# Kernel tuning notes

Measured on AMD Instinct MI355X. Metric: run time of the kernel, lower is better.

The kernel has to match this reference:

```python
import jax, jax.numpy as jnp
import numpy as np

D_HID = 1024
N_HEADS = 16
D_HEAD = D_HID // N_HEADS


def setup_inputs() -> dict:
    key = jax.random.key(0)
    k_x, k_w, k_b = jax.random.split(key, 3)
    x = jax.random.normal(k_x, (8, 4096, D_HID), dtype=jnp.float32)
    # qkv linear params (torch Linear: y = x @ W.T + b; we store W already transposed)
    W_qkv = jax.random.normal(k_w, (D_HID, 3 * D_HID), dtype=jnp.float32) / np.sqrt(D_HID)
    b_qkv = jax.random.normal(k_b, (3 * D_HID,), dtype=jnp.float32) * 0.01
    return {"x": x, "W_qkv": W_qkv, "b_qkv": b_qkv}


def reference(x, W_qkv, b_qkv):
    B, N, _ = x.shape
    qkv = x @ W_qkv + b_qkv  # [B, N, 3*d_hid]
    q, k, v = jnp.split(qkv, 3, axis=-1)

    def heads(t):  # [B, N, d_hid] -> [B, H, N, d_head]
        return t.reshape(B, N, N_HEADS, D_HEAD).transpose(0, 2, 1, 3)

    q, k, v = heads(q), heads(k), heads(v)
    # channel attention: contract over sequence N -> [B, H, d_head, d_head]
    attn = jnp.einsum("bhnd,bhne->bhde", q, k) / np.sqrt(D_HEAD)
    attn = jax.nn.softmax(attn, axis=-1)  # softmax over channel dim
    # outputs = V @ attn : [B, H, N, d_head]
    out = jnp.einsum("bhnd,bhde->bhne", v, attn)
    out = out.transpose(0, 2, 1, 3).reshape(B, N, N_HEADS * D_HEAD)
    return out
```

## Files before the change

### kernel.cpp

```cpp
#include <hip/hip_runtime.h>
#include <hip/hip_bf16.h>


typedef __attribute__((ext_vector_type(4))) float  f32x4;
typedef __attribute__((ext_vector_type(8))) short  bf16x8;
typedef __attribute__((ext_vector_type(8))) unsigned short u16x8;

typedef __attribute__((address_space(1))) const unsigned int GBUF;
typedef __attribute__((address_space(3))) unsigned int       LBUF;

#define DEVI __device__ __forceinline__

static constexpr int BATCH = 8;
static constexpr int NSEQ  = 4096;
static constexpr int DHID  = 1024;
static constexpr int NHEAD = 16;
static constexpr int DH    = 64;
static constexpr int MROWS = BATCH * NSEQ;
static constexpr int N3    = 3 * DHID;

DEVI unsigned short f2bf(float f) {
    unsigned int u = __float_as_uint(f);
    u = (u + 0x7fffu + ((u >> 16) & 1u)) >> 16;
    return (unsigned short)u;
}

__global__ void k_cvt_x(const float* __restrict__ x, unsigned short* __restrict__ xb, int n8) {
    int i = blockIdx.x * 256 + threadIdx.x;
    int stride = gridDim.x * 256;
    for (; i < n8; i += stride) {
        f32x4 a = *(const f32x4*)(x + (size_t)i * 8);
        f32x4 b = *(const f32x4*)(x + (size_t)i * 8 + 4);
        u16x8 r;
#pragma unroll
        for (int j = 0; j < 4; j++) { r[j] = f2bf(a[j]); r[4 + j] = f2bf(b[j]); }
        *(u16x8*)(xb + (size_t)i * 8) = r;
    }
}

__global__ void k_wt(const float* __restrict__ W, unsigned short* __restrict__ Wt) {
    __shared__ float s[32][33];
    int c0 = blockIdx.x * 32;
    int k0 = blockIdx.y * 32;
    int tx = threadIdx.x & 31, ty = threadIdx.x >> 5;
#pragma unroll
    for (int i = 0; i < 4; i++)
        s[ty + 8 * i][tx] = W[(size_t)(k0 + ty + 8 * i) * N3 + c0 + tx];
    __syncthreads();
#pragma unroll
    for (int i = 0; i < 4; i++)
        Wt[(size_t)(c0 + ty + 8 * i) * DHID + k0 + tx] = f2bf(s[tx][ty + 8 * i]);
}

__global__ __launch_bounds__(512, 2) void k_gemm1(
        const unsigned short* __restrict__ xb, const unsigned short* __restrict__ Wt,
        const float* __restrict__ bias,
        unsigned short* __restrict__ Q, unsigned short* __restrict__ Kw,
        unsigned short* __restrict__ V) {
    __shared__ __align__(16) unsigned short As[2][16384];
    __shared__ __align__(16) unsigned short Bs[2][16384];

    int nwg = gridDim.x;
    int cpx = nwg >> 3;
    int id  = blockIdx.x;
    int swz = (id & 7) * cpx + (id >> 3);
    int mt = swz / 12, nt = swz % 12;
    int m0 = mt * 256, n0 = nt * 256;

    int t = threadIdx.x, l = t & 63, w = t >> 6;
    int wr = w >> 2, wc = w & 3;
    int lr = l & 15;

    const unsigned short* aSrc = xb + (size_t)m0 * DHID;
    const unsigned short* bSrc = Wt + (size_t)n0 * DHID;

    int scol = ((t & 7) * 8) ^ (((t >> 3) & 7) << 3);
    int c0 = ((l >> 4) * 8) ^ ((l & 7) << 3);
    int aRow = wr * 128 + lr;
    int bRow = wc * 64 + lr;

#define STAGE_A(bi, kt, h) do { \
        const unsigned short* _s = aSrc + (size_t)((h) * 128 + (t >> 3)) * DHID + (kt) * 64 + scol; \
        unsigned short* _d = &As[bi][(h) * 8192 + t * 8]; \
        __builtin_amdgcn_global_load_lds((GBUF*)_s, (LBUF*)_d, 16, 0, 0); \
        __builtin_amdgcn_global_load_lds((GBUF*)(_s + 64 * DHID), (LBUF*)(_d + 4096), 16, 0, 0); \
    } while (0)
#define STAGE_B(bi, kt, h) do { \
        const unsigned short* _s = bSrc + (size_t)((h) * 128 + (t >> 3)) * DHID + (kt) * 64 + scol; \
        unsigned short* _d = &Bs[bi][(h) * 8192 + t * 8]; \
        __builtin_amdgcn_global_load_lds((GBUF*)_s, (LBUF*)_d, 16, 0, 0); \
        __builtin_amdgcn_global_load_lds((GBUF*)(_s + 64 * DHID), (LBUF*)(_d + 4096), 16, 0, 0); \
    } while (0)
#define LDA(bi, dst, mh) \
    _Pragma("unroll") for (int m2 = 0; m2 < 4; m2++) { \
        const unsigned short* _row = &As[bi][(aRow + (mh) * 64 + m2 * 16) * 64]; \
        dst[m2][0] = *(const bf16x8*)(_row + c0); \
        dst[m2][1] = *(const bf16x8*)(_row + (c0 ^ 32)); \
    }
#define LDB(bi, dst, nh) \
    _Pragma("unroll") for (int n2 = 0; n2 < 2; n2++) { \
        const unsigned short* _row = &Bs[bi][(bRow + (nh) * 32 + n2 * 16) * 64]; \
        dst[n2][0] = *(const bf16x8*)(_row + c0); \
        dst[n2][1] = *(const bf16x8*)(_row + (c0 ^ 32)); \
    }
#define MM(mh, nh, A_, B_) \
    _Pragma("unroll") for (int m2 = 0; m2 < 4; m2++) \
    _Pragma("unroll") for (int n2 = 0; n2 < 2; n2++) { \
        acc[(mh)*4+m2][(nh)*2+n2] = __builtin_amdgcn_mfma_f32_16x16x32_bf16(A_[m2][0], B_[n2][0], acc[(mh)*4+m2][(nh)*2+n2], 0, 0, 0); \
        acc[(mh)*4+m2][(nh)*2+n2] = __builtin_amdgcn_mfma_f32_16x16x32_bf16(A_[m2][1], B_[n2][1], acc[(mh)*4+m2][(nh)*2+n2], 0, 0, 0); \
    }
#define BAR __builtin_amdgcn_s_barrier()
#define LGKM0 do { asm volatile("s_waitcnt lgkmcnt(0)" ::: "memory"); \
                   __builtin_amdgcn_sched_barrier(0); } while (0)
#define VM4 asm volatile("s_waitcnt vmcnt(4)" ::: "memory")
#define VM0 asm volatile("s_waitcnt vmcnt(0)" ::: "memory")
#define PRIO1 __builtin_amdgcn_s_setprio(1)
#define PRIO0 __builtin_amdgcn_s_setprio(0)

    f32x4 acc[8][4] = {};
    bf16x8 fA0[4][2], fA1[4][2], fB0[2][2], fB1[2][2];

    STAGE_A(0, 0, 0); STAGE_A(0, 0, 1);
    STAGE_B(0, 0, 0); STAGE_B(0, 0, 1);
    STAGE_A(1, 1, 0); STAGE_A(1, 1, 1);
    VM4;
    BAR;

#pragma unroll 1
    for (int i = 0; i < 8; ++i) {
        int kc1 = 2 * i + 1;
        int kn0 = (2 * i + 2) & 15, kn1 = (2 * i + 3) & 15;
        LDA(0, fA0, 0); LDB(0, fB0, 0); STAGE_B(1, kc1, 0);
        BAR; LGKM0; PRIO1; MM(0, 0, fA0, fB0); PRIO0; BAR;

        LDA(0, fA1, 1); STAGE_B(1, kc1, 1);
        BAR; LGKM0; PRIO1; MM(1, 0, fA1, fB0); PRIO0; BAR;

        LDB(0, fB1, 1); STAGE_A(0, kn0, 0);
        BAR; LGKM0; PRIO1; MM(1, 1, fA1, fB1); PRIO0; BAR;

        STAGE_A(0, kn0, 1);
        BAR; PRIO1; MM(0, 1, fA0, fB1); PRIO0;
        VM4;
        BAR;
        LDA(1, fA0, 0); LDB(1, fB0, 0); STAGE_B(0, kn0, 0);
        BAR; LGKM0; PRIO1; MM(0, 0, fA0, fB0); PRIO0; BAR;

        LDA(1, fA1, 1); STAGE_B(0, kn0, 1);
        BAR; LGKM0; PRIO1; MM(1, 0, fA1, fB0); PRIO0; BAR;

        LDB(1, fB1, 1); STAGE_A(1, kn1, 0);
        BAR; LGKM0; PRIO1; MM(1, 1, fA1, fB1); PRIO0; BAR;

        STAGE_A(1, kn1, 1);
        BAR; PRIO1; MM(0, 1, fA0, fB1); PRIO0;
        VM4;
        BAR;
    }

    VM0;
    BAR;

    int hg   = nt * 4 + wc;
    int part = hg >> 4;
    int h    = hg & 15;
    unsigned short* dst = (part == 0) ? Q : ((part == 1) ? Kw : V);
    int b   = m0 >> 12;
    int nnb = m0 & 4095;
    unsigned short* dstp = dst + ((size_t)(b * 16 + h) * NSEQ) * DH;

    unsigned short* eb = (w < 4) ? (&As[0][0] + w * 8192) : (&Bs[0][0] + (w - 4) * 8192);

    float bv[4];
#pragma unroll
    for (int n = 0; n < 4; n++) bv[n] = bias[n0 + wc * 64 + n * 16 + lr];

#pragma unroll
    for (int n = 0; n < 4; n++)
#pragma unroll
        for (int m = 0; m < 8; m++)
#pragma unroll
            for (int j = 0; j < 4; j++) {
                int lm = m * 16 + (l >> 4) * 4 + j;
                eb[lm * 64 + ((n * 16 + lr) ^ (((lm >> 2) & 3) << 4))] =
                    f2bf(acc[m][n][j] + bv[n]);
            }

    const size_t base2 = (size_t)(nnb + wr * 128) * DH;
#pragma unroll
    for (int rr = 0; rr < 16; rr++) {
        int u = rr * 64 + l;
        int row = u >> 3, unit = u & 7;
        bf16x8 v = *(const bf16x8*)&eb[row * 64 + ((unit * 8) ^ (((row >> 2) & 3) << 4))];
        *(bf16x8*)(dstp + base2 + (size_t)u * 8) = v;
    }
#undef STAGE_A
#undef STAGE_B
#undef LDA
#undef LDB
#undef MM
#undef BAR
#undef LGKM0
#undef VM4
#undef VM0
#undef PRIO1
#undef PRIO0
}

__global__ __launch_bounds__(256, 2) void k_qk(
        const unsigned short* __restrict__ Q, const unsigned short* __restrict__ K,
        float* __restrict__ part) {
    __shared__ unsigned short Qt[64 * 40];
    __shared__ unsigned short Kt[64 * 40];

    int bid = blockIdx.x;
    int bh = bid >> 2, ch = bid & 3;
    const unsigned short* Qb = Q + ((size_t)bh * NSEQ + ch * 1024) * DH;
    const unsigned short* Kb = K + ((size_t)bh * NSEQ + ch * 1024) * DH;

    int t = threadIdx.x, l = t & 63, w = t >> 6;
    int wr = w >> 1, wc = w & 1;
    int nn = t & 31;
    int dg = t >> 5;

    f32x4 acc[2][2] = {};

    size_t ro0 = (size_t)nn * DH + dg * 8;
    bf16x8 qv = *(const bf16x8*)(Qb + ro0);
    bf16x8 kv = *(const bf16x8*)(Kb + ro0);

    for (int ns = 0; ns < 32; ns++) {
        const size_t rn = (size_t)((((ns + 1) & 31) * 32) + nn) * DH + dg * 8;
        bf16x8 qn = *(const bf16x8*)(Qb + rn);
        bf16x8 kn = *(const bf16x8*)(Kb + rn);
        __syncthreads();
#pragma unroll
        for (int j = 0; j < 8; j++) {
            Qt[(dg * 8 + j) * 40 + nn] = qv[j];
            Kt[(dg * 8 + j) * 40 + nn] = kv[j];
        }
        __syncthreads();
        bf16x8 a[2], b[2];
#pragma unroll
        for (int m = 0; m < 2; m++)
            a[m] = *(const bf16x8*)(Qt + (wr * 32 + m * 16 + (l & 15)) * 40 + (l >> 4) * 8);
#pragma unroll
        for (int n = 0; n < 2; n++)
            b[n] = *(const bf16x8*)(Kt + (wc * 32 + n * 16 + (l & 15)) * 40 + (l >> 4) * 8);
#pragma unroll
        for (int m = 0; m < 2; m++)
#pragma unroll
            for (int n = 0; n < 2; n++)
                acc[m][n] = __builtin_amdgcn_mfma_f32_16x16x32_bf16(a[m], b[n], acc[m][n], 0, 0, 0);
        qv = qn; kv = kn;
    }

    float* P = part + ((size_t)ch * 128 + bh) * 4096;
#pragma unroll
    for (int m = 0; m < 2; m++)
#pragma unroll
        for (int n = 0; n < 2; n++)
#pragma unroll
            for (int j = 0; j < 4; j++) {
                int d = wr * 32 + m * 16 + (l >> 4) * 4 + j;
                int e = wc * 32 + n * 16 + (l & 15);
                P[d * 64 + e] = acc[m][n][j];
            }
}

__global__ void k_softmax(const float* __restrict__ part, unsigned short* __restrict__ attn_t) {
    int bh = blockIdx.x;
    int d  = threadIdx.x;
    const float* p = part + (size_t)bh * 4096 + d * 64;
    const size_t cs = (size_t)128 * 4096;
    float s[64];
#pragma unroll
    for (int e = 0; e < 64; e++)
        s[e] = (p[e] + p[cs + e] + p[2 * cs + e] + p[3 * cs + e]) * 0.125f;
    float mx = s[0];
#pragma unroll
    for (int e = 1; e < 64; e++) mx = fmaxf(mx, s[e]);
    float sum = 0.f;
#pragma unroll
    for (int e = 0; e < 64; e++) { s[e] = __expf(s[e] - mx); sum += s[e]; }
    float inv = 1.f / sum;
    unsigned short* a = attn_t + (size_t)bh * 4096;
#pragma unroll
    for (int e = 0; e < 64; e++)
        a[e * 64 + d] = f2bf(s[e] * inv);
}

__global__ __launch_bounds__(256, 2) void k_out(
        const unsigned short* __restrict__ V, const unsigned short* __restrict__ attn_t,
        float* __restrict__ out) {
    int bid = blockIdx.x;
    int bh = bid >> 4, ntile = bid & 15;
    int b = bh >> 4, h = bh & 15;
    int t = threadIdx.x, l = t & 63, w = t >> 6;
    int r0 = ntile * 256 + w * 64;

    const unsigned short* Vb = V + (size_t)bh * NSEQ * DH;
    const unsigned short* Ab = attn_t + (size_t)bh * 4096;

    bf16x8 bf[4][2];
#pragma unroll
    for (int n = 0; n < 4; n++)
#pragma unroll
        for (int ks = 0; ks < 2; ks++)
            bf[n][ks] = *(const bf16x8*)(Ab + (n * 16 + (l & 15)) * 64 + ks * 32 + (l >> 4) * 8);

    f32x4 acc[4][4] = {};
#pragma unroll
    for (int m = 0; m < 4; m++) {
        const unsigned short* vr = Vb + (size_t)(r0 + m * 16 + (l & 15)) * DH + (l >> 4) * 8;
        bf16x8 av0 = *(const bf16x8*)(vr);
        bf16x8 av1 = *(const bf16x8*)(vr + 32);
#pragma unroll
        for (int n = 0; n < 4; n++) {
            acc[m][n] = __builtin_amdgcn_mfma_f32_16x16x32_bf16(av0, bf[n][0], acc[m][n], 0, 0, 0);
            acc[m][n] = __builtin_amdgcn_mfma_f32_16x16x32_bf16(av1, bf[n][1], acc[m][n], 0, 0, 0);
        }
    }

    float* ob = out + (size_t)b * NSEQ * DHID + (size_t)h * DH;
#pragma unroll
    for (int m = 0; m < 4; m++)
#pragma unroll
        for (int n = 0; n < 4; n++)
#pragma unroll
            for (int j = 0; j < 4; j++) {
                int nn = r0 + m * 16 + (l >> 4) * 4 + j;
                int e  = n * 16 + (l & 15);
                ob[(size_t)nn * DHID + e] = acc[m][n][j];
            }
}

extern "C" void kernel_launch(void* const* d_in, const int* in_sizes, int n_in,
                              void* d_out, int out_size, void* d_ws, size_t ws_size,
                              hipStream_t stream) {
    const float* x    = (const float*)d_in[0];
    const float* W    = (const float*)d_in[1];
    const float* bias = (const float*)d_in[2];
    float* out = (float*)d_out;

    char* wsp = (char*)d_ws;
    unsigned short* xb   = (unsigned short*)(wsp);
    unsigned short* Wt   = (unsigned short*)(wsp + 67108864);
    unsigned short* Qw   = (unsigned short*)(wsp + 73400320);
    unsigned short* Kww  = (unsigned short*)(wsp + 140509184);
    unsigned short* Vw   = (unsigned short*)(wsp + 207618048);
    float*          part = (float*)(wsp + 274726912);
    unsigned short* attn = (unsigned short*)(wsp + 283115520);

    k_cvt_x<<<2048, 256, 0, stream>>>(x, xb, MROWS * DHID / 8);
    k_wt<<<dim3(N3 / 32, DHID / 32), 256, 0, stream>>>(W, Wt);
    k_gemm1<<<(MROWS / 256) * (N3 / 256), 512, 0, stream>>>(xb, Wt, bias, Qw, Kww, Vw);
    k_qk<<<128 * 4, 256, 0, stream>>>(Qw, Kww, part);
    k_softmax<<<128, 64, 0, stream>>>(part, attn);
    k_out<<<128 * 16, 256, 0, stream>>>(Vw, attn, out);
}
```

Baseline: 547.4 us.

## Store Q and K transposed from GEMM epilogue so QK kernel skips LDS transpose

The QKV GEMM epilogue now writes Q and K in a head-major [d_head, N] layout, using a swizzled LDS staging buffer to transpose each tile, while V keeps its original layout. The QK^T kernel then loads MFMA operands straight from global memory along the sequence dimension, dropping its per-iteration LDS transpose and the two barriers per step. This trades the reduction kernel's LDS and sync overhead for strided row writes in the GEMM epilogue and uncached direct global loads in k_qk.

After: 552.2 us. No clear change (+0.9%).

```diff
diff --git a/kernel.cpp b/kernel.cpp
--- a/kernel.cpp
+++ b/kernel.cpp
@@ -5,6 +5,7 @@
 typedef __attribute__((ext_vector_type(4))) float  f32x4;
 typedef __attribute__((ext_vector_type(8))) short  bf16x8;
 typedef __attribute__((ext_vector_type(8))) unsigned short u16x8;
+typedef __attribute__((ext_vector_type(4))) unsigned short u16x4;
 
 typedef __attribute__((address_space(1))) const unsigned int GBUF;
 typedef __attribute__((address_space(3))) unsigned int       LBUF;
@@ -55,7 +56,7 @@
 __global__ __launch_bounds__(512, 2) void k_gemm1(
         const unsigned short* __restrict__ xb, const unsigned short* __restrict__ Wt,
         const float* __restrict__ bias,
-        unsigned short* __restrict__ Q, unsigned short* __restrict__ Kw,
+        unsigned short* __restrict__ Qt, unsigned short* __restrict__ Kt,
         unsigned short* __restrict__ V) {
     __shared__ __align__(16) unsigned short As[2][16384];
     __shared__ __align__(16) unsigned short Bs[2][16384];
@@ -70,12 +71,13 @@
     int t = threadIdx.x, l = t & 63, w = t >> 6;
     int wr = w >> 2, wc = w & 3;
     int lr = l & 15;
+    int hi = l >> 4;
 
     const unsigned short* aSrc = xb + (size_t)m0 * DHID;
     const unsigned short* bSrc = Wt + (size_t)n0 * DHID;
 
     int scol = ((t & 7) * 8) ^ (((t >> 3) & 7) << 3);
-    int c0 = ((l >> 4) * 8) ^ ((l & 7) << 3);
+    int c0 = (hi * 8) ^ ((l & 7) << 3);
     int aRow = wr * 128 + lr;
     int bRow = wc * 64 + lr;
 
@@ -164,10 +166,8 @@
     int hg   = nt * 4 + wc;
     int part = hg >> 4;
     int h    = hg & 15;
-    unsigned short* dst = (part == 0) ? Q : ((part == 1) ? Kw : V);
-    int b   = m0 >> 12;
-    int nnb = m0 & 4095;
-    unsigned short* dstp = dst + ((size_t)(b * 16 + h) * NSEQ) * DH;
+    int b    = m0 >> 12;
+    int nnb  = m0 & 4095;
 
     unsigned short* eb = (w < 4) ? (&As[0][0] + w * 8192) : (&Bs[0][0] + (w - 4) * 8192);
 
@@ -175,24 +175,46 @@
 #pragma unroll
     for (int n = 0; n < 4; n++) bv[n] = bias[n0 + wc * 64 + n * 16 + lr];
 
-#pragma unroll
-    for (int n = 0; n < 4; n++)
-#pragma unroll
-        for (int m = 0; m < 8; m++)
-#pragma unroll
-            for (int j = 0; j < 4; j++) {
-                int lm = m * 16 + (l >> 4) * 4 + j;
-                eb[lm * 64 + ((n * 16 + lr) ^ (((lm >> 2) & 3) << 4))] =
-                    f2bf(acc[m][n][j] + bv[n]);
+    if (part < 2) {
+        unsigned short* dstp = ((part == 0) ? Qt : Kt) + (size_t)(b * 16 + h) * DH * NSEQ;
+#pragma unroll
+        for (int n = 0; n < 4; n++) {
+            int e = n * 16 + lr;
+#pragma unroll
+            for (int m = 0; m < 8; m++) {
+                u16x4 pk;
+#pragma unroll
+                for (int j = 0; j < 4; j++) pk[j] = f2bf(acc[m][n][j] + bv[n]);
+                int u = m * 2 + (hi >> 1);
+                *(u16x4*)((char*)eb + e * 256 + (((u ^ (lr & 7))) << 4) + (hi & 1) * 8) = pk;
             }
-
-    const size_t base2 = (size_t)(nnb + wr * 128) * DH;
-#pragma unroll
-    for (int rr = 0; rr < 16; rr++) {
-        int u = rr * 64 + l;
-        int row = u >> 3, unit = u & 7;
-        bf16x8 v = *(const bf16x8*)&eb[row * 64 + ((unit * 8) ^ (((row >> 2) & 3) << 4))];
-        *(bf16x8*)(dstp + base2 + (size_t)u * 8) = v;
+        }
+#pragma unroll
+        for (int k2 = 0; k2 < 16; k2++) {
+            int er = k2 * 4 + hi;
+            bf16x8 v = *(const bf16x8*)((const char*)eb + er * 256 + ((lr ^ (er & 7)) << 4));
+            *(bf16x8*)(dstp + (size_t)er * NSEQ + nnb + wr * 128 + lr * 8) = v;
+        }
+    } else {
+        unsigned short* dstp = V + (size_t)(b * 16 + h) * NSEQ * DH;
+#pragma unroll
+        for (int n = 0; n < 4; n++)
+#pragma unroll
+            for (int m = 0; m < 8; m++)
+#pragma unroll
+                for (int j = 0; j < 4; j++) {
+                    int lm = m * 16 + hi * 4 + j;
+                    eb[lm * 64 + ((n * 16 + lr) ^ (((lm >> 2) & 3) << 4))] =
+                        f2bf(acc[m][n][j] + bv[n]);
+                }
+        const size_t base2 = (size_t)(nnb + wr * 128) * DH;
+#pragma unroll
+        for (int rr = 0; rr < 16; rr++) {
+            int u = rr * 64 + l;
+            int row = u >> 3, unit = u & 7;
+            bf16x8 v = *(const bf16x8*)&eb[row * 64 + ((unit * 8) ^ (((row >> 2) & 3) << 4))];
+            *(bf16x8*)(dstp + base2 + (size_t)u * 8) = v;
+        }
     }
 #undef STAGE_A
 #undef STAGE_B
@@ -208,51 +230,34 @@
 }
 
 __global__ __launch_bounds__(256, 2) void k_qk(
-        const unsigned short* __restrict__ Q, const unsigned short* __restrict__ K,
+        const unsigned short* __restrict__ Qt, const unsigned short* __restrict__ Kt,
         float* __restrict__ part) {
-    __shared__ unsigned short Qt[64 * 40];
-    __shared__ unsigned short Kt[64 * 40];
-
     int bid = blockIdx.x;
     int bh = bid >> 2, ch = bid & 3;
-    const unsigned short* Qb = Q + ((size_t)bh * NSEQ + ch * 1024) * DH;
-    const unsigned short* Kb = K + ((size_t)bh * NSEQ + ch * 1024) * DH;
+    const unsigned short* Qb = Qt + (size_t)bh * DH * NSEQ + ch * 1024;
+    const unsigned short* Kb = Kt + (size_t)bh * DH * NSEQ + ch * 1024;
 
     int t = threadIdx.x, l = t & 63, w = t >> 6;
-    int wr = w >> 1, wc = w & 1;
-    int nn = t & 31;
-    int dg = t >> 5;
+    int wd = w >> 1, we = w & 1;
+    int lr = l & 15, hi = l >> 4;
 
     f32x4 acc[2][2] = {};
 
-    size_t ro0 = (size_t)nn * DH + dg * 8;
-    bf16x8 qv = *(const bf16x8*)(Qb + ro0);
-    bf16x8 kv = *(const bf16x8*)(Kb + ro0);
-
+#pragma unroll 4
     for (int ns = 0; ns < 32; ns++) {
-        const size_t rn = (size_t)((((ns + 1) & 31) * 32) + nn) * DH + dg * 8;
-        bf16x8 qn = *(const bf16x8*)(Qb + rn);
-        bf16x8 kn = *(const bf16x8*)(Kb + rn);
-        __syncthreads();
-#pragma unroll
-        for (int j = 0; j < 8; j++) {
-            Qt[(dg * 8 + j) * 40 + nn] = qv[j];
-            Kt[(dg * 8 + j) * 40 + nn] = kv[j];
-        }
-        __syncthreads();
+        const int base = ns * 32 + hi * 8;
         bf16x8 a[2], b[2];
 #pragma unroll
         for (int m = 0; m < 2; m++)
-            a[m] = *(const bf16x8*)(Qt + (wr * 32 + m * 16 + (l & 15)) * 40 + (l >> 4) * 8);
+            a[m] = *(const bf16x8*)(Qb + (size_t)(wd * 32 + m * 16 + lr) * NSEQ + base);
 #pragma unroll
         for (int n = 0; n < 2; n++)
-            b[n] = *(const bf16x8*)(Kt + (wc * 32 + n * 16 + (l & 15)) * 40 + (l >> 4) * 8);
+            b[n] = *(const bf16x8*)(Kb + (size_t)(we * 32 + n * 16 + lr) * NSEQ + base);
 #pragma unroll
         for (int m = 0; m < 2; m++)
 #pragma unroll
             for (int n = 0; n < 2; n++)
                 acc[m][n] = __builtin_amdgcn_mfma_f32_16x16x32_bf16(a[m], b[n], acc[m][n], 0, 0, 0);
-        qv = qn; kv = kn;
     }
 
     float* P = part + ((size_t)ch * 128 + bh) * 4096;
@@ -262,8 +267,8 @@
         for (int n = 0; n < 2; n++)
 #pragma unroll
             for (int j = 0; j < 4; j++) {
-                int d = wr * 32 + m * 16 + (l >> 4) * 4 + j;
-                int e = wc * 32 + n * 16 + (l & 15);
+                int d = wd * 32 + m * 16 + hi * 4 + j;
+                int e = we * 32 + n * 16 + lr;
                 P[d * 64 + e] = acc[m][n][j];
             }
 }
```
